# Kernel optimization log

Hardware: AMD Instinct MI355X
Metric: run time of the kernel (lower is better)

Reference implementation:

```python
import jax, jax.numpy as jnp
import numpy as np

B, HGT, WID, D, NS = 4, 64, 128, 128, 2
LN_EPS = 1e-5

def layer_norm(x, g, b):
    m = jnp.mean(x, axis=-1, keepdims=True)
    v = jnp.mean((x - m) ** 2, axis=-1, keepdims=True)
    return (x - m) * jax.lax.rsqrt(v + LN_EPS) * g + b

def setup_inputs() -> dict:
    key = jax.random.key(0)
    ks = jax.random.split(key, 8)
    src = jax.random.normal(ks[0], (B, HGT * WID, D), jnp.float32)
    L = (HGT // NS) * (WID // NS)  # 2048
    s = 0.05
    return {
        "source": src,
        "target": src,  # identical -> self-attention branch in original
        "shifted_window_attn_mask": jax.random.normal(ks[1], (NS * NS, L, L), jnp.float32),
        "shifted_window_attn_mask_1d": jnp.zeros((NS, WID // NS, WID // NS), jnp.float32),
        "height": HGT,
        "width": WID,
        "attn_num_splits": NS,
        "with_shift": 1,
        "Wq": jax.random.normal(ks[2], (D, D), jnp.float32) * s,
        "Wk": jax.random.normal(ks[3], (D, D), jnp.float32) * s,
        "Wv": jax.random.normal(ks[4], (D, D), jnp.float32) * s,
        "Wm": jax.random.normal(ks[5], (D, D), jnp.float32) * s,
        "g1": jnp.ones((D,), jnp.float32),
        "b1": jnp.zeros((D,), jnp.float32),
        "W1": jax.random.normal(ks[6], (2 * D, 8 * D), jnp.float32) * s,
        "W2": jax.random.normal(ks[7], (8 * D, D), jnp.float32) * s,
        "g2": jnp.ones((D,), jnp.float32),
        "b2": jnp.zeros((D,), jnp.float32),
    }

def _shifted_window_self_attn(q, k, v, ns, with_shift, h, w, attn_mask):
    b, _, c = q.shape
    hh, ww = h // ns, w // ns  # window sizes
    sh, sw = hh // 2, ww // 2
    L = hh * ww

    def to_windows(x):
        x = x.reshape(b, h, w, c)
        if with_shift:
            x = jnp.roll(x, shift=(-sh, -sw), axis=(1, 2))
        # (b, ns, hh, ns, ww, c) -> (b*ns*ns, hh*ww, c)
        x = x.reshape(b, ns, hh, ns, ww, c).transpose(0, 1, 3, 2, 4, 5)
        return x.reshape(b * ns * ns, L, c)

    qw, kw, vw = to_windows(q), to_windows(k), to_windows(v)
    scores = jnp.einsum("bqc,bkc->bqk", qw, kw) / (c ** 0.5)  # (b*ns^2, L, L)
    if with_shift:
        scores = (scores.reshape(b, ns * ns, L, L) + attn_mask).reshape(b * ns * ns, L, L)
    attn = jax.nn.softmax(scores, axis=-1)
    out = jnp.einsum("bqk,bkc->bqc", attn, vw)
    # merge windows back
    out = out.reshape(b, ns, ns, hh, ww, c).transpose(0, 1, 3, 2, 4, 5).reshape(b, h, w, c)
    if with_shift:
        out = jnp.roll(out, shift=(sh, sw), axis=(1, 2))
    return out.reshape(b, h * w, c)

def reference(source, target, shifted_window_attn_mask, shifted_window_attn_mask_1d,
              height, width, attn_num_splits, with_shift,
              Wq, Wk, Wv, Wm, g1, b1, W1, W2, g2, b2):
    # target == source -> self-attention, attn_num_splits > 1 -> shifted-window path
    q = source @ Wq
    k = target @ Wk
    v = target @ Wv
    message = _shifted_window_self_attn(q, k, v, attn_num_splits, with_shift,
                                        height, width, shifted_window_attn_mask)
    message = layer_norm(message @ Wm, g1, b1)
    h = jnp.concatenate([source, message], axis=-1)  # (B, HW, 2D)
    message = jax.nn.gelu(h @ W1, approximate=False) @ W2
    message = layer_norm(message, g2, b2)
    return source + message
```

## Files before the change

kernel.cpp:

```cpp
#include <hip/hip_runtime.h>

typedef unsigned short u16;
typedef __bf16 bf16x8 __attribute__((ext_vector_type(8)));
typedef float f32x4 __attribute__((ext_vector_type(4)));

#define MFMA(a, b, c) __builtin_amdgcn_mfma_f32_16x16x32_bf16(a, b, c, 0, 0, 0)


__device__ __forceinline__ u16 f2b(float f) {
  unsigned u = __builtin_bit_cast(unsigned, f);
  u += 0x7fffu + ((u >> 16) & 1u);
  return (u16)(u >> 16);
}
__device__ __forceinline__ float b2f(u16 h) {
  unsigned u = (unsigned)h << 16;
  return __builtin_bit_cast(float, u);
}
__device__ __forceinline__ void glds16(const u16* g, u16* l) {
  __builtin_amdgcn_global_load_lds((const __attribute__((address_space(1))) void*)g,
                                   (__attribute__((address_space(3))) void*)l, 16, 0, 0);
}

#define QW_OFF   ((size_t)0)
#define KW_OFF   ((size_t)8 << 20)
#define VBUF_OFF ((size_t)16 << 20)
#define O1_OFF   ((size_t)24 << 20)
#define O2_OFF   ((size_t)40 << 20)
#define SRCB_OFF ((size_t)64 << 20)
#define MSG1_OFF ((size_t)72 << 20)
#define L1_OFF   ((size_t)80 << 20)
#define L2P_OFF  (((size_t)80 << 20) + 131072)
#define WQT_OFF  (((size_t)80 << 20) + 262144)
#define WKT_OFF  (WQT_OFF + 32768)
#define WVT_OFF  (WQT_OFF + 65536)
#define WMT_OFF  (WQT_OFF + 98304)
#define W1T_OFF  (WQT_OFF + 131072)
#define W2T_OFF  (WQT_OFF + 655360)

__global__ void k_prep(const float* __restrict__ wq, const float* __restrict__ wk,
                       const float* __restrict__ wv, const float* __restrict__ wm,
                       const float* __restrict__ w1, const float* __restrict__ w2,
                       u16* __restrict__ wqt, u16* __restrict__ wkt,
                       u16* __restrict__ wvt, u16* __restrict__ wmt,
                       u16* __restrict__ w1t, u16* __restrict__ w2t) {
  int t = blockIdx.x * 256 + threadIdx.x;
  if (t < 65536) {
    int m = t >> 14, loc = t & 16383;
    int n = loc >> 7, k = loc & 127;
    const float* s = (m == 0) ? wq : (m == 1) ? wk : (m == 2) ? wv : wm;
    u16* d = (m == 0) ? wqt : (m == 1) ? wkt : (m == 2) ? wvt : wmt;
    const float sc = (m == 0) ? 0.08838834764831845f : 1.0f;
    d[n * 128 + k] = f2b(s[k * 128 + n] * sc);
  } else if (t < 65536 + 262144) {
    int loc = t - 65536;
    int n = loc >> 8, k = loc & 255;
    w1t[n * 256 + k] = f2b(w1[k * 1024 + n]);
  } else if (t < 65536 + 262144 + 131072) {
    int loc = t - 327680;
    int n = loc >> 10, k = loc & 1023;
    w2t[n * 1024 + k] = f2b(w2[k * 128 + n]);
  }
}

__global__ __launch_bounds__(256, 2)
void k_qkv(const float* __restrict__ src,
           const u16* __restrict__ wtq, const u16* __restrict__ wtk,
           const u16* __restrict__ wtv,
           u16* __restrict__ qw, u16* __restrict__ kw, u16* __restrict__ vbuf,
           u16* __restrict__ srcb) {
  __shared__ __align__(16) u16 At[64 * 136];
  __shared__ __align__(16) u16 Bt[128 * 136];
  const int tid = threadIdx.x, bid = blockIdx.x;
  const int lane = tid & 63, wid = tid >> 6;
  const int l15 = lane & 15, quad = lane >> 4;

  {
    const int row = tid >> 2, part = tid & 3;
    const int t = bid * 64 + row;
    const int g = t >> 11, p = t & 2047;
    const int b = g >> 2, wi = (g >> 1) & 1, wj = g & 1;
    const int ii = p >> 6, jj = p & 63;
    const int y = (wi * 32 + ii + 16) & 63;
    const int x = (wj * 64 + jj + 32) & 127;
    const int srow = b * 8192 + y * 128 + x;
    const float4* sp = (const float4*)(src + srow * 128) + part * 8;
    u16* lp = &At[row * 136 + part * 32];
    u16* gp = srcb + srow * 128 + part * 32;
#pragma unroll
    for (int q = 0; q < 8; ++q) {
      float4 v = sp[q];
      ushort4 h = make_ushort4(f2b(v.x), f2b(v.y), f2b(v.z), f2b(v.w));
      *(ushort4*)(lp + q * 4) = h;
      *(ushort4*)(gp + q * 4) = h;
    }
  }
  __syncthreads();

  bf16x8 afrag[4];
  const int arow = wid * 16 + l15;
#pragma unroll
  for (int kk = 0; kk < 4; ++kk)
    afrag[kk] = *(const bf16x8*)&At[arow * 136 + kk * 32 + quad * 8];

  const f32x4 fz = {0.f, 0.f, 0.f, 0.f};
#pragma unroll 1
  for (int m = 0; m < 3; ++m) {
    const u16* wp = (m == 0) ? wtq : (m == 1) ? wtk : wtv;
    {
      const int n = tid >> 1, half = tid & 1;
      const uint4* sp = (const uint4*)(wp + n * 128 + half * 64);
      uint4* dp = (uint4*)&Bt[n * 136 + half * 64];
#pragma unroll
      for (int q = 0; q < 8; ++q) dp[q] = sp[q];
    }
    __syncthreads();
    f32x4 acc[8];
#pragma unroll
    for (int nt = 0; nt < 8; ++nt) acc[nt] = fz;
#pragma unroll
    for (int kk = 0; kk < 4; ++kk) {
#pragma unroll
      for (int nt = 0; nt < 8; ++nt) {
        bf16x8 bfr = *(const bf16x8*)&Bt[(nt * 16 + l15) * 136 + kk * 32 + quad * 8];
        acc[nt] = MFMA(afrag[kk], bfr, acc[nt]);
      }
    }
    const int t0 = bid * 64 + wid * 16 + quad * 4;
    if (m < 2) {
      u16* dst = (m == 0) ? qw : kw;
#pragma unroll
      for (int nt = 0; nt < 8; ++nt) {
        const int d = nt * 16 + l15;
#pragma unroll
        for (int r = 0; r < 4; ++r) dst[(t0 + r) * 128 + d] = f2b(acc[nt][r]);
      }
    } else {
      const int g = bid >> 5;
      const int p0 = t0 & 2047;
#pragma unroll
      for (int nt = 0; nt < 8; ++nt) {
        const int d = nt * 16 + l15;
        ushort4 hv = make_ushort4(f2b(acc[nt][0]), f2b(acc[nt][1]),
                                  f2b(acc[nt][2]), f2b(acc[nt][3]));
        *(ushort4*)&vbuf[g * 262144 + d * 2048 + p0] = hv;
      }
    }
    __syncthreads();
  }
}

__global__ __launch_bounds__(256, 2)
void k_attn(const u16* __restrict__ qw, const u16* __restrict__ kw,
            const u16* __restrict__ vbuf, const float* __restrict__ mask,
            u16* __restrict__ o1, u16* __restrict__ o2,
            float* __restrict__ l1, float* __restrict__ l2) {
  __shared__ __align__(16) u16 Kt[2][64 * 128];
  __shared__ __align__(16) u16 Vt[2][128 * 64];
  __shared__ __align__(16) u16 Pt[128 * 40];
  const int tid = threadIdx.x;
  const int bid = (blockIdx.x & 7) * 64 + (blockIdx.x >> 3);
  const int lane = tid & 63, wid = tid >> 6;
  const int l15 = lane & 15, quad = lane >> 4;
  const int b = bid & 3, w = (bid >> 2) & 3, half = (bid >> 4) & 1, qb = bid >> 5;
  const int g = b * 4 + w;
  const int k0 = half * 1024;
  const u16* kbase = kw + g * 262144 + k0 * 128;
  const u16* vbase = vbuf + g * 262144 + k0;
  const int qrow0 = qb * 128 + wid * 32;
  const float* mlane = mask + (size_t)w * 4194304 + (size_t)(qrow0 + quad * 4) * 2048 + k0 + l15;

  int offk[4], offv[4], dstb[4];
#pragma unroll
  for (int j = 0; j < 4; ++j) {
    const int s = wid * 256 + j * 64 + lane;
    const int rk = s >> 4, bk = (s & 15) ^ (rk & 15);
    offk[j] = rk * 128 + bk * 8;
    const int dv = s >> 3, bv = (s & 7) ^ (dv & 7);
    offv[j] = dv * 2048 + bv * 8;
    dstb[j] = (wid * 256 + j * 64) * 8;
  }

  bf16x8 qfrag[2][4];
#pragma unroll
  for (int qs = 0; qs < 2; ++qs) {
    const u16* qp = qw + g * 262144 + (qrow0 + qs * 16 + l15) * 128 + quad * 8;
#pragma unroll
    for (int kk = 0; kk < 4; ++kk) qfrag[qs][kk] = *(const bf16x8*)(qp + kk * 32);
  }
  const f32x4 fz = {0.f, 0.f, 0.f, 0.f};
  f32x4 o[2][8];
#pragma unroll
  for (int qs = 0; qs < 2; ++qs)
#pragma unroll
    for (int nt = 0; nt < 8; ++nt) o[qs][nt] = fz;
  float lr[2][4] = {{0.f, 0.f, 0.f, 0.f}, {0.f, 0.f, 0.f, 0.f}};
  const float L2E = 1.4426950408889634f;

#pragma unroll
  for (int j = 0; j < 4; ++j) {
    glds16(kbase + offk[j], &Kt[0][dstb[j]]);
    glds16(vbase + offv[j], &Vt[0][dstb[j]]);
  }
  float mpf[16];
#pragma unroll
  for (int qs = 0; qs < 2; ++qs)
#pragma unroll
    for (int ntl = 0; ntl < 2; ++ntl)
#pragma unroll
      for (int r = 0; r < 4; ++r)
        mpf[qs * 8 + ntl * 4 + r] = mlane[(qs * 16 + r) * 2048 + ntl * 16];

#pragma unroll 1
  for (int kt = 0; kt < 16; ++kt) {
    const int p = kt & 1;
    __syncthreads();
    if (kt < 15) {
      const u16* kb = kbase + (kt + 1) * 8192;
      const u16* vb = vbase + (kt + 1) * 64;
#pragma unroll
      for (int j = 0; j < 4; ++j) {
        glds16(kb + offk[j], &Kt[p ^ 1][dstb[j]]);
        glds16(vb + offv[j], &Vt[p ^ 1][dstb[j]]);
      }
    }
#pragma unroll
    for (int ks = 0; ks < 2; ++ks) {
      float mn[16];
      const bool hasn = (kt < 15) || (ks == 0);
      const int ncol = kt * 64 + 32 + ks * 32;
      if (hasn) {
#pragma unroll
        for (int qs = 0; qs < 2; ++qs)
#pragma unroll
          for (int ntl = 0; ntl < 2; ++ntl)
#pragma unroll
            for (int r = 0; r < 4; ++r)
              mn[qs * 8 + ntl * 4 + r] = mlane[(qs * 16 + r) * 2048 + ncol + ntl * 16];
      }
      f32x4 s[2][2];
#pragma unroll
      for (int qs = 0; qs < 2; ++qs)
#pragma unroll
        for (int ntl = 0; ntl < 2; ++ntl)
#pragma unroll
          for (int r = 0; r < 4; ++r) s[qs][ntl][r] = mpf[qs * 8 + ntl * 4 + r];
#pragma unroll
      for (int kk = 0; kk < 4; ++kk)
#pragma unroll
        for (int ntl = 0; ntl < 2; ++ntl) {
          bf16x8 kfr = *(const bf16x8*)&Kt[p][(ks * 32 + ntl * 16 + l15) * 128 +
                                             (((kk * 4 + quad) ^ l15) * 8)];
          s[0][ntl] = MFMA(qfrag[0][kk], kfr, s[0][ntl]);
          s[1][ntl] = MFMA(qfrag[1][kk], kfr, s[1][ntl]);
        }
#pragma unroll
      for (int qs = 0; qs < 2; ++qs)
#pragma unroll
        for (int ntl = 0; ntl < 2; ++ntl)
#pragma unroll
          for (int r = 0; r < 4; ++r) {
            const float pv = exp2f(s[qs][ntl][r] * L2E);
            lr[qs][r] += pv;
            Pt[(wid * 32 + qs * 16 + quad * 4 + r) * 40 + ntl * 16 + l15] = f2b(pv);
          }
      bf16x8 pf0 = *(const bf16x8*)&Pt[(wid * 32 + l15) * 40 + quad * 8];
      bf16x8 pf1 = *(const bf16x8*)&Pt[(wid * 32 + 16 + l15) * 40 + quad * 8];
#pragma unroll
      for (int nt = 0; nt < 8; ++nt) {
        bf16x8 vfr = *(const bf16x8*)&Vt[p][(nt * 16 + l15) * 64 +
                                            (((ks * 4 + quad) ^ (l15 & 7)) * 8)];
        o[0][nt] = MFMA(pf0, vfr, o[0][nt]);
        o[1][nt] = MFMA(pf1, vfr, o[1][nt]);
      }
      if (hasn) {
#pragma unroll
        for (int i = 0; i < 16; ++i) mpf[i] = mn[i];
      }
    }
  }

#pragma unroll
  for (int off = 1; off < 16; off <<= 1)
#pragma unroll
    for (int qs = 0; qs < 2; ++qs)
#pragma unroll
      for (int r = 0; r < 4; ++r) lr[qs][r] += __shfl_xor(lr[qs][r], off, 16);
  u16* op = half ? o2 : o1;
  float* lp = half ? l2 : l1;
#pragma unroll
  for (int qs = 0; qs < 2; ++qs) {
    const int t0 = g * 2048 + qrow0 + qs * 16 + quad * 4;
#pragma unroll
    for (int r = 0; r < 4; ++r) {
      const float inv = 1.f / lr[qs][r];
#pragma unroll
      for (int nt = 0; nt < 8; ++nt)
        op[(size_t)(t0 + r) * 128 + nt * 16 + l15] = f2b(o[qs][nt][r] * inv);
      if (l15 == 0) lp[t0 + r] = lr[qs][r];
    }
  }
}

__global__ __launch_bounds__(256, 2)
void k_wmln(const u16* __restrict__ o1, const u16* __restrict__ o2,
            const float* __restrict__ l1, const float* __restrict__ l2,
            const u16* __restrict__ wmt, const float* __restrict__ g1,
            const float* __restrict__ b1, u16* __restrict__ msg1) {
  __shared__ __align__(16) u16 At[64 * 136];
  __shared__ __align__(16) u16 Bt[128 * 136];
  const int tid = threadIdx.x, bid = blockIdx.x;
  const int lane = tid & 63, wid = tid >> 6;
  const int l15 = lane & 15, quad = lane >> 4;
  {
    const int row = tid >> 2, part = tid & 3;
    const int m = bid * 64 + row;
    const float la = l1[m], lb = l2[m];
    const float wA = la / (la + lb), wB = lb / (la + lb);
    const u16* p1 = o1 + (size_t)m * 128 + part * 32;
    const u16* p2 = o2 + (size_t)m * 128 + part * 32;
    u16* lp = &At[row * 136 + part * 32];
#pragma unroll
    for (int q = 0; q < 4; ++q) {
      ushort4 xa = *(const ushort4*)(p1 + q * 8);
      ushort4 xb = *(const ushort4*)(p1 + q * 8 + 4);
      ushort4 ya = *(const ushort4*)(p2 + q * 8);
      ushort4 yb = *(const ushort4*)(p2 + q * 8 + 4);
      ushort4 ha = make_ushort4(f2b(b2f(xa.x) * wA + b2f(ya.x) * wB),
                                f2b(b2f(xa.y) * wA + b2f(ya.y) * wB),
                                f2b(b2f(xa.z) * wA + b2f(ya.z) * wB),
                                f2b(b2f(xa.w) * wA + b2f(ya.w) * wB));
      ushort4 hb = make_ushort4(f2b(b2f(xb.x) * wA + b2f(yb.x) * wB),
                                f2b(b2f(xb.y) * wA + b2f(yb.y) * wB),
                                f2b(b2f(xb.z) * wA + b2f(yb.z) * wB),
                                f2b(b2f(xb.w) * wA + b2f(yb.w) * wB));
      *(ushort4*)(lp + q * 8) = ha;
      *(ushort4*)(lp + q * 8 + 4) = hb;
    }
  }
  {
    const int n = tid >> 1, half = tid & 1;
    const uint4* sp = (const uint4*)(wmt + n * 128 + half * 64);
    uint4* dp = (uint4*)&Bt[n * 136 + half * 64];
#pragma unroll
    for (int q = 0; q < 8; ++q) dp[q] = sp[q];
  }
  __syncthreads();
  bf16x8 afrag[4];
  const int arow = wid * 16 + l15;
#pragma unroll
  for (int kk = 0; kk < 4; ++kk)
    afrag[kk] = *(const bf16x8*)&At[arow * 136 + kk * 32 + quad * 8];
  const f32x4 fz = {0.f, 0.f, 0.f, 0.f};
  f32x4 acc[8];
#pragma unroll
  for (int nt = 0; nt < 8; ++nt) acc[nt] = fz;
#pragma unroll
  for (int kk = 0; kk < 4; ++kk)
#pragma unroll
    for (int nt = 0; nt < 8; ++nt) {
      bf16x8 bfr = *(const bf16x8*)&Bt[(nt * 16 + l15) * 136 + kk * 32 + quad * 8];
      acc[nt] = MFMA(afrag[kk], bfr, acc[nt]);
    }
  float sum[4] = {0, 0, 0, 0}, sq[4] = {0, 0, 0, 0};
#pragma unroll
  for (int nt = 0; nt < 8; ++nt)
#pragma unroll
    for (int r = 0; r < 4; ++r) {
      const float v = acc[nt][r];
      sum[r] += v;
      sq[r] += v * v;
    }
#pragma unroll
  for (int off = 1; off < 16; off <<= 1)
#pragma unroll
    for (int r = 0; r < 4; ++r) {
      sum[r] += __shfl_xor(sum[r], off, 16);
      sq[r] += __shfl_xor(sq[r], off, 16);
    }
  float mean[4], rstd[4];
#pragma unroll
  for (int r = 0; r < 4; ++r) {
    mean[r] = sum[r] * (1.f / 128.f);
    const float var = sq[r] * (1.f / 128.f) - mean[r] * mean[r];
    rstd[r] = rsqrtf(var + 1e-5f);
  }
  const int t0 = bid * 64 + wid * 16 + quad * 4;
#pragma unroll
  for (int nt = 0; nt < 8; ++nt) {
    const int d = nt * 16 + l15;
    const float gg = g1[d], bb = b1[d];
#pragma unroll
    for (int r = 0; r < 4; ++r) {
      const int tt = t0 + r;
      msg1[(size_t)tt * 128 + d] = f2b((acc[nt][r] - mean[r]) * rstd[r] * gg + bb);
    }
  }
}

__global__ __launch_bounds__(256, 2)
void k_mlp(const u16* __restrict__ srcb, const u16* __restrict__ msg1,
           const u16* __restrict__ w1t, const u16* __restrict__ w2t,
           const float* __restrict__ g2, const float* __restrict__ b2,
           const float* __restrict__ src, float* __restrict__ out) {
  __shared__ __align__(16) u16 Bt1[2][32 * 256];
  __shared__ __align__(16) u16 Bt2[2][128 * 32];
  __shared__ __align__(16) u16 Ht[64 * 40];
  const int tid = threadIdx.x, bid = blockIdx.x;
  const int lane = tid & 63, wid = tid >> 6;
  const int l15 = lane & 15, quad = lane >> 4;

  int off1[4], db1[4], off2[2], db2[2];
#pragma unroll
  for (int j = 0; j < 4; ++j) {
    const int s = wid * 256 + j * 64 + lane;
    const int r = s >> 5, c = s & 31;
    off1[j] = r * 256 + (c ^ (r & 15)) * 8;
    db1[j] = (wid * 256 + j * 64) * 8;
  }
#pragma unroll
  for (int j = 0; j < 2; ++j) {
    const int s = wid * 128 + j * 64 + lane;
    const int r = s >> 2, c = s & 3;
    off2[j] = r * 1024 + (c ^ (r & 3)) * 8;
    db2[j] = (wid * 128 + j * 64) * 8;
  }

  bf16x8 afrag[8];
  {
    const int t_sp = bid * 64 + wid * 16 + l15;
    const u16* sp = srcb + (size_t)t_sp * 128 + quad * 8;
    const int bb = t_sp >> 13, rem = t_sp & 8191;
    const int y = rem >> 7, x = rem & 127;
    const int u = (y + 48) & 63, v = (x + 96) & 127;
    const int wrow = (bb * 4 + (u >> 5) * 2 + (v >> 6)) * 2048 + (u & 31) * 64 + (v & 63);
    const u16* mp = msg1 + (size_t)wrow * 128 + quad * 8;
#pragma unroll
    for (int kk = 0; kk < 4; ++kk) {
      afrag[kk] = *(const bf16x8*)(sp + kk * 32);
      afrag[kk + 4] = *(const bf16x8*)(mp + kk * 32);
    }
  }
  const f32x4 fz = {0.f, 0.f, 0.f, 0.f};
  f32x4 oacc[8];
#pragma unroll
  for (int nt = 0; nt < 8; ++nt) oacc[nt] = fz;

#pragma unroll
  for (int j = 0; j < 4; ++j) glds16(w1t + off1[j], &Bt1[0][db1[j]]);
#pragma unroll
  for (int j = 0; j < 2; ++j) glds16(w2t + off2[j], &Bt2[0][db2[j]]);

#pragma unroll 1
  for (int hc = 0; hc < 32; ++hc) {
    const int p = hc & 1;
    __syncthreads();
    if (hc < 31) {
#pragma unroll
      for (int j = 0; j < 4; ++j)
        glds16(w1t + (hc + 1) * 8192 + off1[j], &Bt1[p ^ 1][db1[j]]);
#pragma unroll
      for (int j = 0; j < 2; ++j)
        glds16(w2t + (hc + 1) * 32 + off2[j], &Bt2[p ^ 1][db2[j]]);
    }

    f32x4 hacc[2];
    hacc[0] = fz;
    hacc[1] = fz;
#pragma unroll
    for (int kk = 0; kk < 8; ++kk)
#pragma unroll
      for (int nt = 0; nt < 2; ++nt) {
        bf16x8 b1fr = *(const bf16x8*)&Bt1[p][(nt * 16 + l15) * 256 +
                                             (((kk * 4 + quad) ^ l15) * 8)];
        hacc[nt] = MFMA(afrag[kk], b1fr, hacc[nt]);
      }
#pragma unroll
    for (int nt = 0; nt < 2; ++nt)
#pragma unroll
      for (int r = 0; r < 4; ++r) {
        const float x = hacc[nt][r];
        const float y = 0.5f * x * (1.f + erff(x * 0.70710678118654752f));
        Ht[(wid * 16 + quad * 4 + r) * 40 + nt * 16 + l15] = f2b(y);
      }
    bf16x8 hf = *(const bf16x8*)&Ht[(wid * 16 + l15) * 40 + quad * 8];
#pragma unroll
    for (int nt = 0; nt < 8; ++nt) {
      bf16x8 b2fr = *(const bf16x8*)&Bt2[p][(nt * 16 + l15) * 32 +
                                           ((quad ^ (l15 & 3)) * 8)];
      oacc[nt] = MFMA(hf, b2fr, oacc[nt]);
    }
  }

  float sum[4] = {0, 0, 0, 0}, sq[4] = {0, 0, 0, 0};
#pragma unroll
  for (int nt = 0; nt < 8; ++nt)
#pragma unroll
    for (int r = 0; r < 4; ++r) {
      const float v = oacc[nt][r];
      sum[r] += v;
      sq[r] += v * v;
    }
#pragma unroll
  for (int off = 1; off < 16; off <<= 1)
#pragma unroll
    for (int r = 0; r < 4; ++r) {
      sum[r] += __shfl_xor(sum[r], off, 16);
      sq[r] += __shfl_xor(sq[r], off, 16);
    }
  float mean[4], rstd[4];
#pragma unroll
  for (int r = 0; r < 4; ++r) {
    mean[r] = sum[r] * (1.f / 128.f);
    const float var = sq[r] * (1.f / 128.f) - mean[r] * mean[r];
    rstd[r] = rsqrtf(var + 1e-5f);
  }
  const int t0 = bid * 64 + wid * 16 + quad * 4;
#pragma unroll
  for (int nt = 0; nt < 8; ++nt) {
    const int d = nt * 16 + l15;
    const float gg = g2[d], bb = b2[d];
#pragma unroll
    for (int r = 0; r < 4; ++r) {
      const int idx = (t0 + r) * 128 + d;
      out[idx] = src[idx] + (oacc[nt][r] - mean[r]) * rstd[r] * gg + bb;
    }
  }
}

extern "C" void kernel_launch(void* const* d_in, const int* in_sizes, int n_in,
                              void* d_out, int out_size, void* d_ws, size_t ws_size,
                              hipStream_t stream) {
  const float* src  = (const float*)d_in[0];
  const float* mask = (const float*)d_in[2];
  const float* Wq = (const float*)d_in[8];
  const float* Wk = (const float*)d_in[9];
  const float* Wv = (const float*)d_in[10];
  const float* Wm = (const float*)d_in[11];
  const float* g1 = (const float*)d_in[12];
  const float* b1 = (const float*)d_in[13];
  const float* W1 = (const float*)d_in[14];
  const float* W2 = (const float*)d_in[15];
  const float* g2 = (const float*)d_in[16];
  const float* b2 = (const float*)d_in[17];
  char* ws = (char*)d_ws;
  u16* qw   = (u16*)(ws + QW_OFF);
  u16* kw   = (u16*)(ws + KW_OFF);
  u16* vbuf = (u16*)(ws + VBUF_OFF);
  u16* o1   = (u16*)(ws + O1_OFF);
  u16* o2   = (u16*)(ws + O2_OFF);
  float* l1 = (float*)(ws + L1_OFF);
  float* l2 = (float*)(ws + L2P_OFF);
  u16* srcb = (u16*)(ws + SRCB_OFF);
  u16* msg1 = (u16*)(ws + MSG1_OFF);
  u16* wqt = (u16*)(ws + WQT_OFF);
  u16* wkt = (u16*)(ws + WKT_OFF);
  u16* wvt = (u16*)(ws + WVT_OFF);
  u16* wmt = (u16*)(ws + WMT_OFF);
  u16* w1t = (u16*)(ws + W1T_OFF);
  u16* w2t = (u16*)(ws + W2T_OFF);

  k_prep<<<1792, 256, 0, stream>>>(Wq, Wk, Wv, Wm, W1, W2, wqt, wkt, wvt, wmt, w1t, w2t);
  k_qkv<<<512, 256, 0, stream>>>(src, wqt, wkt, wvt, qw, kw, vbuf, srcb);
  k_attn<<<512, 256, 0, stream>>>(qw, kw, vbuf, mask, o1, o2, l1, l2);
  k_wmln<<<512, 256, 0, stream>>>(o1, o2, l1, l2, wmt, g1, b1, msg1);
  k_mlp<<<512, 256, 0, stream>>>(srcb, msg1, w1t, w2t, g2, b2, src, (float*)d_out);
}
```

Before: 295.6 us.

## Split QKV projection across blocks and prefetch attention mask a tile ahead

The QKV kernel now launches three times as many blocks, each computing only one of Q, K or V for its 64-row tile instead of looping over all three. This adds parallelism and removes the per-matrix syncs, but each block re-reads and re-converts the fp32 source rows. In the attention kernel, the 64 mask columns for the next key tile are loaded once per tile, right after the next K/V prefetch is issued, instead of per 32-column half-step. That doubles the mask registers held. Launch bounds for k_qkv and k_wmln are raised to 3 blocks per CU to allow higher occupancy.

```diff
diff --git a/kernel.cpp b/kernel.cpp
--- a/kernel.cpp
+++ b/kernel.cpp
@@ -62,7 +62,7 @@
   }
 }
 
-__global__ __launch_bounds__(256, 2)
+__global__ __launch_bounds__(256, 3)
 void k_qkv(const float* __restrict__ src,
            const u16* __restrict__ wtq, const u16* __restrict__ wtk,
            const u16* __restrict__ wtv,
@@ -70,7 +70,8 @@
            u16* __restrict__ srcb) {
   __shared__ __align__(16) u16 At[64 * 136];
   __shared__ __align__(16) u16 Bt[128 * 136];
-  const int tid = threadIdx.x, bid = blockIdx.x;
+  const int tid = threadIdx.x, bid0 = blockIdx.x;
+  const int bid = bid0 / 3, m = bid0 - bid * 3;
   const int lane = tid & 63, wid = tid >> 6;
   const int l15 = lane & 15, quad = lane >> 4;
 
@@ -91,8 +92,16 @@
       float4 v = sp[q];
       ushort4 h = make_ushort4(f2b(v.x), f2b(v.y), f2b(v.z), f2b(v.w));
       *(ushort4*)(lp + q * 4) = h;
-      *(ushort4*)(gp + q * 4) = h;
-    }
+      if (m == 0) *(ushort4*)(gp + q * 4) = h;
+    }
+  }
+  {
+    const u16* wp = (m == 0) ? wtq : (m == 1) ? wtk : wtv;
+    const int n = tid >> 1, half = tid & 1;
+    const uint4* sp = (const uint4*)(wp + n * 128 + half * 64);
+    uint4* dp = (uint4*)&Bt[n * 136 + half * 64];
+#pragma unroll
+    for (int q = 0; q < 8; ++q) dp[q] = sp[q];
   }
   __syncthreads();
 
@@ -103,49 +112,36 @@
     afrag[kk] = *(const bf16x8*)&At[arow * 136 + kk * 32 + quad * 8];
 
   const f32x4 fz = {0.f, 0.f, 0.f, 0.f};
-#pragma unroll 1
-  for (int m = 0; m < 3; ++m) {
-    const u16* wp = (m == 0) ? wtq : (m == 1) ? wtk : wtv;
-    {
-      const int n = tid >> 1, half = tid & 1;
-      const uint4* sp = (const uint4*)(wp + n * 128 + half * 64);
-      uint4* dp = (uint4*)&Bt[n * 136 + half * 64];
-#pragma unroll
-      for (int q = 0; q < 8; ++q) dp[q] = sp[q];
-    }
-    __syncthreads();
-    f32x4 acc[8];
-#pragma unroll
-    for (int nt = 0; nt < 8; ++nt) acc[nt] = fz;
-#pragma unroll
-    for (int kk = 0; kk < 4; ++kk) {
-#pragma unroll
-      for (int nt = 0; nt < 8; ++nt) {
-        bf16x8 bfr = *(const bf16x8*)&Bt[(nt * 16 + l15) * 136 + kk * 32 + quad * 8];
-        acc[nt] = MFMA(afrag[kk], bfr, acc[nt]);
-      }
-    }
-    const int t0 = bid * 64 + wid * 16 + quad * 4;
-    if (m < 2) {
-      u16* dst = (m == 0) ? qw : kw;
-#pragma unroll
-      for (int nt = 0; nt < 8; ++nt) {
-        const int d = nt * 16 + l15;
-#pragma unroll
-        for (int r = 0; r < 4; ++r) dst[(t0 + r) * 128 + d] = f2b(acc[nt][r]);
-      }
-    } else {
-      const int g = bid >> 5;
-      const int p0 = t0 & 2047;
-#pragma unroll
-      for (int nt = 0; nt < 8; ++nt) {
-        const int d = nt * 16 + l15;
-        ushort4 hv = make_ushort4(f2b(acc[nt][0]), f2b(acc[nt][1]),
-                                  f2b(acc[nt][2]), f2b(acc[nt][3]));
-        *(ushort4*)&vbuf[g * 262144 + d * 2048 + p0] = hv;
-      }
-    }
-    __syncthreads();
+  f32x4 acc[8];
+#pragma unroll
+  for (int nt = 0; nt < 8; ++nt) acc[nt] = fz;
+#pragma unroll
+  for (int kk = 0; kk < 4; ++kk) {
+#pragma unroll
+    for (int nt = 0; nt < 8; ++nt) {
+      bf16x8 bfr = *(const bf16x8*)&Bt[(nt * 16 + l15) * 136 + kk * 32 + quad * 8];
+      acc[nt] = MFMA(afrag[kk], bfr, acc[nt]);
+    }
+  }
+  const int t0 = bid * 64 + wid * 16 + quad * 4;
+  if (m < 2) {
+    u16* dst = (m == 0) ? qw : kw;
+#pragma unroll
+    for (int nt = 0; nt < 8; ++nt) {
+      const int d = nt * 16 + l15;
+#pragma unroll
+      for (int r = 0; r < 4; ++r) dst[(t0 + r) * 128 + d] = f2b(acc[nt][r]);
+    }
+  } else {
+    const int g = bid >> 5;
+    const int p0 = t0 & 2047;
+#pragma unroll
+    for (int nt = 0; nt < 8; ++nt) {
+      const int d = nt * 16 + l15;
+      ushort4 hv = make_ushort4(f2b(acc[nt][0]), f2b(acc[nt][1]),
+                                f2b(acc[nt][2]), f2b(acc[nt][3]));
+      *(ushort4*)&vbuf[g * 262144 + d * 2048 + p0] = hv;
+    }
   }
 }
 
@@ -201,14 +197,14 @@
     glds16(kbase + offk[j], &Kt[0][dstb[j]]);
     glds16(vbase + offv[j], &Vt[0][dstb[j]]);
   }
-  float mpf[16];
+  float mt[32], mtn[32];
 #pragma unroll
   for (int qs = 0; qs < 2; ++qs)
 #pragma unroll
-    for (int ntl = 0; ntl < 2; ++ntl)
+    for (int j = 0; j < 4; ++j)
 #pragma unroll
       for (int r = 0; r < 4; ++r)
-        mpf[qs * 8 + ntl * 4 + r] = mlane[(qs * 16 + r) * 2048 + ntl * 16];
+        mt[qs * 16 + j * 4 + r] = mlane[(qs * 16 + r) * 2048 + j * 16];
 
 #pragma unroll 1
   for (int kt = 0; kt < 16; ++kt) {
@@ -222,28 +218,25 @@
         glds16(kb + offk[j], &Kt[p ^ 1][dstb[j]]);
         glds16(vb + offv[j], &Vt[p ^ 1][dstb[j]]);
       }
+#pragma unroll
+      for (int qs = 0; qs < 2; ++qs)
+#pragma unroll
+        for (int j = 0; j < 4; ++j)
+#pragma unroll
+          for (int r = 0; r < 4; ++r)
+            mtn[qs * 16 + j * 4 + r] =
+                mlane[(qs * 16 + r) * 2048 + (kt + 1) * 64 + j * 16];
     }
 #pragma unroll
     for (int ks = 0; ks < 2; ++ks) {
-      float mn[16];
-      const bool hasn = (kt < 15) || (ks == 0);
-      const int ncol = kt * 64 + 32 + ks * 32;
-      if (hasn) {
-#pragma unroll
-        for (int qs = 0; qs < 2; ++qs)
-#pragma unroll
-          for (int ntl = 0; ntl < 2; ++ntl)
-#pragma unroll
-            for (int r = 0; r < 4; ++r)
-              mn[qs * 8 + ntl * 4 + r] = mlane[(qs * 16 + r) * 2048 + ncol + ntl * 16];
-      }
       f32x4 s[2][2];
 #pragma unroll
       for (int qs = 0; qs < 2; ++qs)
 #pragma unroll
         for (int ntl = 0; ntl < 2; ++ntl)
 #pragma unroll
-          for (int r = 0; r < 4; ++r) s[qs][ntl][r] = mpf[qs * 8 + ntl * 4 + r];
+          for (int r = 0; r < 4; ++r)
+            s[qs][ntl][r] = mt[qs * 16 + (ks * 2 + ntl) * 4 + r];
 #pragma unroll
       for (int kk = 0; kk < 4; ++kk)
 #pragma unroll
@@ -272,10 +265,10 @@
         o[0][nt] = MFMA(pf0, vfr, o[0][nt]);
         o[1][nt] = MFMA(pf1, vfr, o[1][nt]);
       }
-      if (hasn) {
-#pragma unroll
-        for (int i = 0; i < 16; ++i) mpf[i] = mn[i];
-      }
+    }
+    if (kt < 15) {
+#pragma unroll
+      for (int i = 0; i < 32; ++i) mt[i] = mtn[i];
     }
   }
 
@@ -301,7 +294,7 @@
   }
 }
 
-__global__ __launch_bounds__(256, 2)
+__global__ __launch_bounds__(256, 3)
 void k_wmln(const u16* __restrict__ o1, const u16* __restrict__ o2,
             const float* __restrict__ l1, const float* __restrict__ l2,
             const u16* __restrict__ wmt, const float* __restrict__ g1,
@@ -560,7 +553,7 @@
   u16* w2t = (u16*)(ws + W2T_OFF);
 
   k_prep<<<1792, 256, 0, stream>>>(Wq, Wk, Wv, Wm, W1, W2, wqt, wkt, wvt, wmt, w1t, w2t);
-  k_qkv<<<512, 256, 0, stream>>>(src, wqt, wkt, wvt, qw, kw, vbuf, srcb);
+  k_qkv<<<1536, 256, 0, stream>>>(src, wqt, wkt, wvt, qw, kw, vbuf, srcb);
   k_attn<<<512, 256, 0, stream>>>(qw, kw, vbuf, mask, o1, o2, l1, l2);
   k_wmln<<<512, 256, 0, stream>>>(o1, o2, l1, l2, wmt, g1, b1, msg1);
   k_mlp<<<512, 256, 0, stream>>>(srcb, msg1, w1t, w2t, g2, b2, src, (float*)d_out);
```

After: 313.4 us. 6.0% more time.

## Fuse Wm projection and LayerNorm into the MLP kernel

Applied to the files above, without the earlier changes.

Merges the k_wmln kernel into k_mlp. Each block gathers its 64 tokens' attention outputs through the shifted-window index, combines the two halves, applies Wm and LayerNorm in registers and LDS, and feeds the result straight into the MLP A-fragments. This removes one kernel launch and the bf16 msg1 round-trip through global memory. LDS is aliased between the Wm stage and the W1/W2 double buffers, so it needs an extra barrier, and the earlier gather of o1/o2 rows becomes scattered by the window permutation.

```diff
diff --git a/kernel.cpp b/kernel.cpp
--- a/kernel.cpp
+++ b/kernel.cpp
@@ -27,7 +27,6 @@
 #define O1_OFF   ((size_t)24 << 20)
 #define O2_OFF   ((size_t)40 << 20)
 #define SRCB_OFF ((size_t)64 << 20)
-#define MSG1_OFF ((size_t)72 << 20)
 #define L1_OFF   ((size_t)80 << 20)
 #define L2P_OFF  (((size_t)80 << 20) + 131072)
 #define WQT_OFF  (((size_t)80 << 20) + 262144)
@@ -302,23 +301,45 @@
 }
 
 __global__ __launch_bounds__(256, 2)
-void k_wmln(const u16* __restrict__ o1, const u16* __restrict__ o2,
-            const float* __restrict__ l1, const float* __restrict__ l2,
-            const u16* __restrict__ wmt, const float* __restrict__ g1,
-            const float* __restrict__ b1, u16* __restrict__ msg1) {
-  __shared__ __align__(16) u16 At[64 * 136];
-  __shared__ __align__(16) u16 Bt[128 * 136];
+void k_mlp(const u16* __restrict__ o1, const u16* __restrict__ o2,
+           const float* __restrict__ l1, const float* __restrict__ l2,
+           const u16* __restrict__ wmt, const float* __restrict__ g1,
+           const float* __restrict__ b1,
+           const u16* __restrict__ srcb,
+           const u16* __restrict__ w1t, const u16* __restrict__ w2t,
+           const float* __restrict__ g2, const float* __restrict__ b2,
+           const float* __restrict__ src, float* __restrict__ out) {
+  __shared__ __align__(16) u16 lds[27136];
+  u16* Mt  = lds;
+  u16* BtW = lds + 8704;
+  u16* Bt1 = lds;
+  u16* Bt2 = lds + 16384;
+  u16* Ht  = lds + 24576;
   const int tid = threadIdx.x, bid = blockIdx.x;
   const int lane = tid & 63, wid = tid >> 6;
   const int l15 = lane & 15, quad = lane >> 4;
+  const f32x4 fz = {0.f, 0.f, 0.f, 0.f};
+
+  bf16x8 afrag[8];
+  {
+    const int t_sp = bid * 64 + wid * 16 + l15;
+    const u16* sp = srcb + (size_t)t_sp * 128 + quad * 8;
+#pragma unroll
+    for (int kk = 0; kk < 4; ++kk) afrag[kk] = *(const bf16x8*)(sp + kk * 32);
+  }
+
   {
     const int row = tid >> 2, part = tid & 3;
-    const int m = bid * 64 + row;
-    const float la = l1[m], lb = l2[m];
+    const int t_sp = bid * 64 + row;
+    const int bb = t_sp >> 13, rem = t_sp & 8191;
+    const int y = rem >> 7, x = rem & 127;
+    const int u = (y + 48) & 63, v = (x + 96) & 127;
+    const int wrow = (bb * 4 + (u >> 5) * 2 + (v >> 6)) * 2048 + (u & 31) * 64 + (v & 63);
+    const float la = l1[wrow], lb = l2[wrow];
     const float wA = la / (la + lb), wB = lb / (la + lb);
-    const u16* p1 = o1 + (size_t)m * 128 + part * 32;
-    const u16* p2 = o2 + (size_t)m * 128 + part * 32;
-    u16* lp = &At[row * 136 + part * 32];
+    const u16* p1 = o1 + (size_t)wrow * 128 + part * 32;
+    const u16* p2 = o2 + (size_t)wrow * 128 + part * 32;
+    u16* lp = &Mt[row * 136 + part * 32];
 #pragma unroll
     for (int q = 0; q < 4; ++q) {
       ushort4 xa = *(const ushort4*)(p1 + q * 8);
@@ -340,74 +361,65 @@
   {
     const int n = tid >> 1, half = tid & 1;
     const uint4* sp = (const uint4*)(wmt + n * 128 + half * 64);
-    uint4* dp = (uint4*)&Bt[n * 136 + half * 64];
+    uint4* dp = (uint4*)&BtW[n * 136 + half * 64];
 #pragma unroll
     for (int q = 0; q < 8; ++q) dp[q] = sp[q];
   }
   __syncthreads();
-  bf16x8 afrag[4];
-  const int arow = wid * 16 + l15;
-#pragma unroll
-  for (int kk = 0; kk < 4; ++kk)
-    afrag[kk] = *(const bf16x8*)&At[arow * 136 + kk * 32 + quad * 8];
-  const f32x4 fz = {0.f, 0.f, 0.f, 0.f};
-  f32x4 acc[8];
-#pragma unroll
-  for (int nt = 0; nt < 8; ++nt) acc[nt] = fz;
-#pragma unroll
-  for (int kk = 0; kk < 4; ++kk)
+
+  {
+    const int arow = wid * 16 + l15;
+    bf16x8 am[4];
+#pragma unroll
+    for (int kk = 0; kk < 4; ++kk)
+      am[kk] = *(const bf16x8*)&Mt[arow * 136 + kk * 32 + quad * 8];
+    f32x4 acc[8];
+#pragma unroll
+    for (int nt = 0; nt < 8; ++nt) acc[nt] = fz;
+#pragma unroll
+    for (int kk = 0; kk < 4; ++kk)
+#pragma unroll
+      for (int nt = 0; nt < 8; ++nt) {
+        bf16x8 bfr = *(const bf16x8*)&BtW[(nt * 16 + l15) * 136 + kk * 32 + quad * 8];
+        acc[nt] = MFMA(am[kk], bfr, acc[nt]);
+      }
+    float sum[4] = {0, 0, 0, 0}, sq[4] = {0, 0, 0, 0};
+#pragma unroll
+    for (int nt = 0; nt < 8; ++nt)
+#pragma unroll
+      for (int r = 0; r < 4; ++r) {
+        const float v = acc[nt][r];
+        sum[r] += v;
+        sq[r] += v * v;
+      }
+#pragma unroll
+    for (int off = 1; off < 16; off <<= 1)
+#pragma unroll
+      for (int r = 0; r < 4; ++r) {
+        sum[r] += __shfl_xor(sum[r], off, 16);
+        sq[r] += __shfl_xor(sq[r], off, 16);
+      }
+    float mean[4], rstd[4];
+#pragma unroll
+    for (int r = 0; r < 4; ++r) {
+      mean[r] = sum[r] * (1.f / 128.f);
+      const float var = sq[r] * (1.f / 128.f) - mean[r] * mean[r];
+      rstd[r] = rsqrtf(var + 1e-5f);
+    }
 #pragma unroll
     for (int nt = 0; nt < 8; ++nt) {
-      bf16x8 bfr = *(const bf16x8*)&Bt[(nt * 16 + l15) * 136 + kk * 32 + quad * 8];
-      acc[nt] = MFMA(afrag[kk], bfr, acc[nt]);
-    }
-  float sum[4] = {0, 0, 0, 0}, sq[4] = {0, 0, 0, 0};
-#pragma unroll
-  for (int nt = 0; nt < 8; ++nt)
-#pragma unroll
-    for (int r = 0; r < 4; ++r) {
-      const float v = acc[nt][r];
-      sum[r] += v;
-      sq[r] += v * v;
-    }
-#pragma unroll
-  for (int off = 1; off < 16; off <<= 1)
-#pragma unroll
-    for (int r = 0; r < 4; ++r) {
-      sum[r] += __shfl_xor(sum[r], off, 16);
-      sq[r] += __shfl_xor(sq[r], off, 16);
-    }
-  float mean[4], rstd[4];
-#pragma unroll
-  for (int r = 0; r < 4; ++r) {
-    mean[r] = sum[r] * (1.f / 128.f);
-    const float var = sq[r] * (1.f / 128.f) - mean[r] * mean[r];
-    rstd[r] = rsqrtf(var + 1e-5f);
-  }
-  const int t0 = bid * 64 + wid * 16 + quad * 4;
-#pragma unroll
-  for (int nt = 0; nt < 8; ++nt) {
-    const int d = nt * 16 + l15;
-    const float gg = g1[d], bb = b1[d];
-#pragma unroll
-    for (int r = 0; r < 4; ++r) {
-      const int tt = t0 + r;
-      msg1[(size_t)tt * 128 + d] = f2b((acc[nt][r] - mean[r]) * rstd[r] * gg + bb);
-    }
-  }
-}
-
-__global__ __launch_bounds__(256, 2)
-void k_mlp(const u16* __restrict__ srcb, const u16* __restrict__ msg1,
-           const u16* __restrict__ w1t, const u16* __restrict__ w2t,
-           const float* __restrict__ g2, const float* __restrict__ b2,
-           const float* __restrict__ src, float* __restrict__ out) {
-  __shared__ __align__(16) u16 Bt1[2][32 * 256];
-  __shared__ __align__(16) u16 Bt2[2][128 * 32];
-  __shared__ __align__(16) u16 Ht[64 * 40];
-  const int tid = threadIdx.x, bid = blockIdx.x;
-  const int lane = tid & 63, wid = tid >> 6;
-  const int l15 = lane & 15, quad = lane >> 4;
+      const int d = nt * 16 + l15;
+      const float gg = g1[d], bb = b1[d];
+#pragma unroll
+      for (int r = 0; r < 4; ++r)
+        Mt[(wid * 16 + quad * 4 + r) * 136 + d] =
+            f2b((acc[nt][r] - mean[r]) * rstd[r] * gg + bb);
+    }
+#pragma unroll
+    for (int kk = 0; kk < 4; ++kk)
+      afrag[kk + 4] = *(const bf16x8*)&Mt[arow * 136 + kk * 32 + quad * 8];
+  }
+  __syncthreads();
 
   int off1[4], db1[4], off2[2], db2[2];
 #pragma unroll
@@ -424,31 +436,14 @@
     off2[j] = r * 1024 + (c ^ (r & 3)) * 8;
     db2[j] = (wid * 128 + j * 64) * 8;
   }
-
-  bf16x8 afrag[8];
-  {
-    const int t_sp = bid * 64 + wid * 16 + l15;
-    const u16* sp = srcb + (size_t)t_sp * 128 + quad * 8;
-    const int bb = t_sp >> 13, rem = t_sp & 8191;
-    const int y = rem >> 7, x = rem & 127;
-    const int u = (y + 48) & 63, v = (x + 96) & 127;
-    const int wrow = (bb * 4 + (u >> 5) * 2 + (v >> 6)) * 2048 + (u & 31) * 64 + (v & 63);
-    const u16* mp = msg1 + (size_t)wrow * 128 + quad * 8;
-#pragma unroll
-    for (int kk = 0; kk < 4; ++kk) {
-      afrag[kk] = *(const bf16x8*)(sp + kk * 32);
-      afrag[kk + 4] = *(const bf16x8*)(mp + kk * 32);
-    }
-  }
-  const f32x4 fz = {0.f, 0.f, 0.f, 0.f};
   f32x4 oacc[8];
 #pragma unroll
   for (int nt = 0; nt < 8; ++nt) oacc[nt] = fz;
 
 #pragma unroll
-  for (int j = 0; j < 4; ++j) glds16(w1t + off1[j], &Bt1[0][db1[j]]);
-#pragma unroll
-  for (int j = 0; j < 2; ++j) glds16(w2t + off2[j], &Bt2[0][db2[j]]);
+  for (int j = 0; j < 4; ++j) glds16(w1t + off1[j], &Bt1[db1[j]]);
+#pragma unroll
+  for (int j = 0; j < 2; ++j) glds16(w2t + off2[j], &Bt2[db2[j]]);
 
 #pragma unroll 1
   for (int hc = 0; hc < 32; ++hc) {
@@ -457,10 +452,10 @@
     if (hc < 31) {
 #pragma unroll
       for (int j = 0; j < 4; ++j)
-        glds16(w1t + (hc + 1) * 8192 + off1[j], &Bt1[p ^ 1][db1[j]]);
+        glds16(w1t + (hc + 1) * 8192 + off1[j], &Bt1[((p ^ 1) * 8192) + db1[j]]);
 #pragma unroll
       for (int j = 0; j < 2; ++j)
-        glds16(w2t + (hc + 1) * 32 + off2[j], &Bt2[p ^ 1][db2[j]]);
+        glds16(w2t + (hc + 1) * 32 + off2[j], &Bt2[((p ^ 1) * 4096) + db2[j]]);
     }
 
     f32x4 hacc[2];
@@ -470,8 +465,8 @@
     for (int kk = 0; kk < 8; ++kk)
 #pragma unroll
       for (int nt = 0; nt < 2; ++nt) {
-        bf16x8 b1fr = *(const bf16x8*)&Bt1[p][(nt * 16 + l15) * 256 +
-                                             (((kk * 4 + quad) ^ l15) * 8)];
+        bf16x8 b1fr = *(const bf16x8*)&Bt1[p * 8192 + (nt * 16 + l15) * 256 +
+                                           (((kk * 4 + quad) ^ l15) * 8)];
         hacc[nt] = MFMA(afrag[kk], b1fr, hacc[nt]);
       }
 #pragma unroll
@@ -485,8 +480,8 @@
     bf16x8 hf = *(const bf16x8*)&Ht[(wid * 16 + l15) * 40 + quad * 8];
 #pragma unroll
     for (int nt = 0; nt < 8; ++nt) {
-      bf16x8 b2fr = *(const bf16x8*)&Bt2[p][(nt * 16 + l15) * 32 +
-                                           ((quad ^ (l15 & 3)) * 8)];
+      bf16x8 b2fr = *(const bf16x8*)&Bt2[p * 4096 + (nt * 16 + l15) * 32 +
+                                         ((quad ^ (l15 & 3)) * 8)];
       oacc[nt] = MFMA(hf, b2fr, oacc[nt]);
     }
   }
@@ -551,7 +546,6 @@
   float* l1 = (float*)(ws + L1_OFF);
   float* l2 = (float*)(ws + L2P_OFF);
   u16* srcb = (u16*)(ws + SRCB_OFF);
-  u16* msg1 = (u16*)(ws + MSG1_OFF);
   u16* wqt = (u16*)(ws + WQT_OFF);
   u16* wkt = (u16*)(ws + WKT_OFF);
   u16* wvt = (u16*)(ws + WVT_OFF);
@@ -562,6 +556,6 @@
   k_prep<<<1792, 256, 0, stream>>>(Wq, Wk, Wv, Wm, W1, W2, wqt, wkt, wvt, wmt, w1t, w2t);
   k_qkv<<<512, 256, 0, stream>>>(src, wqt, wkt, wvt, qw, kw, vbuf, srcb);
   k_attn<<<512, 256, 0, stream>>>(qw, kw, vbuf, mask, o1, o2, l1, l2);
-  k_wmln<<<512, 256, 0, stream>>>(o1, o2, l1, l2, wmt, g1, b1, msg1);
-  k_mlp<<<512, 256, 0, stream>>>(srcb, msg1, w1t, w2t, g2, b2, src, (float*)d_out);
-}
+  k_mlp<<<512, 256, 0, stream>>>(o1, o2, l1, l2, wmt, g1, b1, srcb, w1t, w2t,
+                                 g2, b2, src, (float*)d_out);
+}
```

Result: faster. 287.5 us (-2.8%).
